# Optimization experiments

Hardware: AMD Instinct MI355X
Metric: run time of the kernel (lower is better)

## Reference

```python
import jax, jax.numpy as jnp
import numpy as np


def setup_inputs() -> dict:
    key = jax.random.key(0)
    k1, k2 = jax.random.split(key)
    BATCH, SLOTS = 64, 65536   # 64 ciphertexts, 2^16 CKKS slots each
    NUM_T = 16                 # number of BSGS diagonal transforms (shifts 2^0..2^15)
    x = jax.random.normal(k1, (BATCH, SLOTS), dtype=jnp.float32)
    diagonals = jax.random.normal(k2, (NUM_T, SLOTS), dtype=jnp.float32)
    return {"x": x, "diagonals": diagonals, "stride": 1, "reps": 1}


def reference(x, diagonals, stride, reps):
    """FHE BSGS conv-as-linear-transform: rotate / plaintext-multiply / accumulate.

    Mirrors LinearTransform.evaluate_transforms:
      for i: out += roll(x, -2**i * stride) * diagonals[i]
      (two rescales are scale-management no-ops numerically)
      final conv roll by slots // (2 * reps).
    """
    slots = x.shape[-1]
    num_t = diagonals.shape[0]
    # Vectorize the rotations: gather all shifted copies at once.
    # shift for transform i is -2**i * stride (roll left by 2**i*stride).
    shifts = (2 ** jnp.arange(num_t, dtype=jnp.int32)) * stride        # [T]
    base = jnp.arange(slots, dtype=jnp.int32)                          # [S]
    idx = (base[None, :] + shifts[:, None]) % slots                    # [T, S] roll(-s) gather
    rolled = x[:, idx]                                                 # [B, T, S]
    out = jnp.einsum('bts,ts->bs', rolled, diagonals)                  # accumulate products
    # final conv roll: roll(slots // (2*reps)) => shift right
    out = jnp.roll(out, slots // (2 * reps), axis=-1)
    return out
```

## Files before the change

kernel.cpp:

```cpp
#include <hip/hip_runtime.h>


#define SLOTS 65536
#define MASK  65535

__global__ __launch_bounds__(256) void bsgs_kernel(
    const float* __restrict__ x,
    const float* __restrict__ diag,
    float* __restrict__ out)
{
    const int b = blockIdx.y;
    const int j = (blockIdx.x * 256 + threadIdx.x) * 4;
    const float* __restrict__ xb = x + (size_t)b * SLOTS;

    float4 acc = make_float4(0.f, 0.f, 0.f, 0.f);

    const float4 vA = *(const float4*)(xb + j);
    const float4 vB = *(const float4*)(xb + ((j + 4) & MASK));

    {
        float4 d = *(const float4*)(diag + 0 * SLOTS + j);
        acc.x += vA.y * d.x; acc.y += vA.z * d.y; acc.z += vA.w * d.z; acc.w += vB.x * d.w;
    }
    {
        float4 d = *(const float4*)(diag + 1 * SLOTS + j);
        acc.x += vA.z * d.x; acc.y += vA.w * d.y; acc.z += vB.x * d.z; acc.w += vB.y * d.w;
    }
    {
        float4 d = *(const float4*)(diag + 2 * SLOTS + j);
        acc.x += vB.x * d.x; acc.y += vB.y * d.y; acc.z += vB.z * d.z; acc.w += vB.w * d.w;
    }
#pragma unroll
    for (int t = 3; t < 16; ++t) {
        const int shift = 1 << t;
        float4 v = *(const float4*)(xb + ((j + shift) & MASK));
        float4 d = *(const float4*)(diag + t * SLOTS + j);
        acc.x += v.x * d.x; acc.y += v.y * d.y; acc.z += v.z * d.z; acc.w += v.w * d.w;
    }

    *(float4*)(out + (size_t)b * SLOTS + (j ^ 32768)) = acc;
}

extern "C" void kernel_launch(void* const* d_in, const int* in_sizes, int n_in,
                              void* d_out, int out_size, void* d_ws, size_t ws_size,
                              hipStream_t stream) {
    const float* x    = (const float*)d_in[0];
    const float* diag = (const float*)d_in[1];
    float* out        = (float*)d_out;

    dim3 grid(SLOTS / (256 * 4), 64);
    bsgs_kernel<<<grid, dim3(256), 0, stream>>>(x, diag, out);
}
```

Baseline: 90.89 us.

## Cache diagonals in registers across batches and stage shifted x windows in LDS

```diff
diff --git a/kernel.cpp b/kernel.cpp
--- a/kernel.cpp
+++ b/kernel.cpp
@@ -3,42 +3,63 @@
 
 #define SLOTS 65536
 #define MASK  65535
+#define CTILE 1024
+#define NB    8
+#define XFOOT 7168
 
 __global__ __launch_bounds__(256) void bsgs_kernel(
     const float* __restrict__ x,
     const float* __restrict__ diag,
     float* __restrict__ out)
 {
-    const int b = blockIdx.y;
-    const int j = (blockIdx.x * 256 + threadIdx.x) * 4;
-    const float* __restrict__ xb = x + (size_t)b * SLOTS;
+    __shared__ float ldsx[XFOOT];
+    const int tid = threadIdx.x;
+    const int c   = blockIdx.x * CTILE;
+    const int bg  = blockIdx.y * NB;
+    const int jj  = tid * 4;
 
-    float4 acc = make_float4(0.f, 0.f, 0.f, 0.f);
+    float4 dreg[16];
+#pragma unroll
+    for (int t = 0; t < 16; ++t)
+        dreg[t] = *(const float4*)(diag + t * SLOTS + c + jj);
 
-    const float4 vA = *(const float4*)(xb + j);
-    const float4 vB = *(const float4*)(xb + ((j + 4) & MASK));
+    for (int b = 0; b < NB; ++b) {
+        const float* __restrict__ xb = x + (size_t)(bg + b) * SLOTS;
 
-    {
-        float4 d = *(const float4*)(diag + 0 * SLOTS + j);
-        acc.x += vA.y * d.x; acc.y += vA.z * d.y; acc.z += vA.w * d.z; acc.w += vB.x * d.w;
+        __syncthreads();
+#pragma unroll
+        for (int k = 0; k < 3; ++k) {
+            const int o = (tid + k * 256) * 4;
+            *(float4*)(ldsx + o) = *(const float4*)(xb + ((c + o) & MASK));
+        }
+#pragma unroll
+        for (int s = 0; s < 4; ++s) {
+            *(float4*)(ldsx + 3072 + s * 1024 + jj) =
+                *(const float4*)(xb + ((c + (4096 << s) + jj) & MASK));
+        }
+        __syncthreads();
+
+        float4 acc = make_float4(0.f, 0.f, 0.f, 0.f);
+        const float4 vA = *(const float4*)(ldsx + jj);
+        const float4 vB = *(const float4*)(ldsx + jj + 4);
+
+        acc.x += vA.y*dreg[0].x; acc.y += vA.z*dreg[0].y; acc.z += vA.w*dreg[0].z; acc.w += vB.x*dreg[0].w;
+        acc.x += vA.z*dreg[1].x; acc.y += vA.w*dreg[1].y; acc.z += vB.x*dreg[1].z; acc.w += vB.y*dreg[1].w;
+        acc.x += vB.x*dreg[2].x; acc.y += vB.y*dreg[2].y; acc.z += vB.z*dreg[2].z; acc.w += vB.w*dreg[2].w;
+#pragma unroll
+        for (int t = 3; t <= 11; ++t) {
+            const float4 v = *(const float4*)(ldsx + jj + (1 << t));
+            acc.x += v.x*dreg[t].x; acc.y += v.y*dreg[t].y; acc.z += v.z*dreg[t].z; acc.w += v.w*dreg[t].w;
+        }
+#pragma unroll
+        for (int s = 0; s < 4; ++s) {
+            const int t = 12 + s;
+            const float4 v = *(const float4*)(ldsx + 3072 + s * 1024 + jj);
+            acc.x += v.x*dreg[t].x; acc.y += v.y*dreg[t].y; acc.z += v.z*dreg[t].z; acc.w += v.w*dreg[t].w;
+        }
+
+        *(float4*)(out + (size_t)(bg + b) * SLOTS + ((c + jj) ^ 32768)) = acc;
     }
-    {
-        float4 d = *(const float4*)(diag + 1 * SLOTS + j);
-        acc.x += vA.z * d.x; acc.y += vA.w * d.y; acc.z += vB.x * d.z; acc.w += vB.y * d.w;
-    }
-    {
-        float4 d = *(const float4*)(diag + 2 * SLOTS + j);
-        acc.x += vB.x * d.x; acc.y += vB.y * d.y; acc.z += vB.z * d.z; acc.w += vB.w * d.w;
-    }
-#pragma unroll
-    for (int t = 3; t < 16; ++t) {
-        const int shift = 1 << t;
-        float4 v = *(const float4*)(xb + ((j + shift) & MASK));
-        float4 d = *(const float4*)(diag + t * SLOTS + j);
-        acc.x += v.x * d.x; acc.y += v.y * d.y; acc.z += v.z * d.z; acc.w += v.w * d.w;
-    }
-
-    *(float4*)(out + (size_t)b * SLOTS + (j ^ 32768)) = acc;
 }
 
 extern "C" void kernel_launch(void* const* d_in, const int* in_sizes, int n_in,
@@ -48,6 +69,6 @@
     const float* diag = (const float*)d_in[1];
     float* out        = (float*)d_out;
 
-    dim3 grid(SLOTS / (256 * 4), 64);
+    dim3 grid(SLOTS / CTILE, 64 / NB);
     bsgs_kernel<<<grid, dim3(256), 0, stream>>>(x, diag, out);
 }
```

After: 85.06 us. -6.4%, faster.

## Process four batches per thread to reuse diagonal loads

Applied to the files above, without the earlier changes.

```diff
diff --git a/kernel.cpp b/kernel.cpp
--- a/kernel.cpp
+++ b/kernel.cpp
@@ -3,42 +3,56 @@
 
 #define SLOTS 65536
 #define MASK  65535
+#define NB    4
 
 __global__ __launch_bounds__(256) void bsgs_kernel(
     const float* __restrict__ x,
     const float* __restrict__ diag,
     float* __restrict__ out)
 {
-    const int b = blockIdx.y;
-    const int j = (blockIdx.x * 256 + threadIdx.x) * 4;
-    const float* __restrict__ xb = x + (size_t)b * SLOTS;
+    const int bid  = blockIdx.x;
+    const int y    = bid & 15;
+    const int xidx = bid >> 4;
+    const int j    = xidx * 1024 + threadIdx.x * 4;
+    const int bg   = y * NB;
 
-    float4 acc = make_float4(0.f, 0.f, 0.f, 0.f);
+    const float* __restrict__ xb = x + (size_t)bg * SLOTS;
 
-    const float4 vA = *(const float4*)(xb + j);
-    const float4 vB = *(const float4*)(xb + ((j + 4) & MASK));
+    float4 acc[NB];
+#pragma unroll
+    for (int b = 0; b < NB; ++b) acc[b] = make_float4(0.f, 0.f, 0.f, 0.f);
 
     {
-        float4 d = *(const float4*)(diag + 0 * SLOTS + j);
-        acc.x += vA.y * d.x; acc.y += vA.z * d.y; acc.z += vA.w * d.z; acc.w += vB.x * d.w;
+        const float4 d0 = *(const float4*)(diag + 0 * SLOTS + j);
+        const float4 d1 = *(const float4*)(diag + 1 * SLOTS + j);
+        const float4 d2 = *(const float4*)(diag + 2 * SLOTS + j);
+#pragma unroll
+        for (int b = 0; b < NB; ++b) {
+            const float* xr = xb + (size_t)b * SLOTS;
+            const float4 vA = *(const float4*)(xr + j);
+            const float4 vB = *(const float4*)(xr + ((j + 4) & MASK));
+            acc[b].x += vA.y * d0.x + vA.z * d1.x + vB.x * d2.x;
+            acc[b].y += vA.z * d0.y + vA.w * d1.y + vB.y * d2.y;
+            acc[b].z += vA.w * d0.z + vB.x * d1.z + vB.z * d2.z;
+            acc[b].w += vB.x * d0.w + vB.y * d1.w + vB.w * d2.w;
+        }
     }
-    {
-        float4 d = *(const float4*)(diag + 1 * SLOTS + j);
-        acc.x += vA.z * d.x; acc.y += vA.w * d.y; acc.z += vB.x * d.z; acc.w += vB.y * d.w;
-    }
-    {
-        float4 d = *(const float4*)(diag + 2 * SLOTS + j);
-        acc.x += vB.x * d.x; acc.y += vB.y * d.y; acc.z += vB.z * d.z; acc.w += vB.w * d.w;
-    }
+
 #pragma unroll
     for (int t = 3; t < 16; ++t) {
-        const int shift = 1 << t;
-        float4 v = *(const float4*)(xb + ((j + shift) & MASK));
-        float4 d = *(const float4*)(diag + t * SLOTS + j);
-        acc.x += v.x * d.x; acc.y += v.y * d.y; acc.z += v.z * d.z; acc.w += v.w * d.w;
+        const float4 d = *(const float4*)(diag + t * SLOTS + j);
+        const int o = (j + (1 << t)) & MASK;
+#pragma unroll
+        for (int b = 0; b < NB; ++b) {
+            const float4 v = *(const float4*)(xb + (size_t)b * SLOTS + o);
+            acc[b].x += v.x * d.x; acc[b].y += v.y * d.y;
+            acc[b].z += v.z * d.z; acc[b].w += v.w * d.w;
+        }
     }
 
-    *(float4*)(out + (size_t)b * SLOTS + (j ^ 32768)) = acc;
+#pragma unroll
+    for (int b = 0; b < NB; ++b)
+        *(float4*)(out + (size_t)(bg + b) * SLOTS + (j ^ 32768)) = acc[b];
 }
 
 extern "C" void kernel_launch(void* const* d_in, const int* in_sizes, int n_in,
@@ -48,6 +62,5 @@
     const float* diag = (const float*)d_in[1];
     float* out        = (float*)d_out;
 
-    dim3 grid(SLOTS / (256 * 4), 64);
-    bsgs_kernel<<<grid, dim3(256), 0, stream>>>(x, diag, out);
+    bsgs_kernel<<<dim3(1024), dim3(256), 0, stream>>>(x, diag, out);
 }
```

Result: faster. 86.38 us (-5.0%).
